# Kernel tuning notes

Measured on AMD Instinct MI355X. Metric: run time of the kernel, lower is better.

## Reference

```python
import jax, jax.numpy as jnp
import numpy as np

WS = 8        # window_size
HEADS = 6     # num_heads
DIM = 96      # dim


def _relative_position_index(ws):
    # Static int index table, identical to the torch buffer construction.
    coords = np.stack(np.meshgrid(np.arange(ws), np.arange(ws), indexing='ij'))  # (2, ws, ws)
    cf = coords.reshape(2, -1)                              # (2, N)
    rel = cf[:, :, None] - cf[:, None, :]                   # (2, N, N)
    rel = rel.transpose(1, 2, 0).copy()                     # (N, N, 2)
    rel[:, :, 0] += ws - 1
    rel[:, :, 1] += ws - 1
    rel[:, :, 0] *= 2 * ws - 1
    return rel.sum(-1)                                      # (N, N)


def setup_inputs() -> dict:
    key = jax.random.key(0)
    ks = jax.random.split(key, 6)
    B, C, H, W = 1, DIM, 512, 512
    return {
        'x': jax.random.normal(ks[0], (B, C, H, W), jnp.float32),
        'qkv_w': jax.random.normal(ks[1], (3 * C, C), jnp.float32) * 0.02,
        'qkv_b': jnp.zeros((3 * C,), jnp.float32),
        'dw_w': jax.random.normal(ks[2], (3 * C, 1, 3, 3), jnp.float32) * 0.02,
        'dw_b': jnp.zeros((3 * C,), jnp.float32),
        'proj_w': jax.random.normal(ks[3], (C, C), jnp.float32) * 0.02,
        'proj_b': jnp.zeros((C,), jnp.float32),
        'temperature': jnp.ones((HEADS, 1, 1), jnp.float32),
        'rel_bias_table': jax.random.normal(ks[4], ((2 * WS - 1) ** 2, HEADS), jnp.float32) * 0.02,
    }


def reference(x, qkv_w, qkv_b, dw_w, dw_b, proj_w, proj_b, temperature, rel_bias_table):
    B, C, H, W = x.shape
    ws, heads = WS, HEADS
    N = ws * ws
    hd = C // heads
    scale = hd ** (-0.5)

    # ---- window partition: (B,C,H,W) -> (B*nW, C, ws, ws) ----
    xw = x.reshape(B, C, H // ws, ws, W // ws, ws)
    xw = xw.transpose(0, 2, 4, 1, 3, 5).reshape(-1, C, ws, ws)

    # ---- qkv 1x1 conv + depthwise 3x3 conv ----
    qkv = jnp.einsum('oi,bihw->bohw', qkv_w, xw) + qkv_b[None, :, None, None]
    qkv = jax.lax.conv_general_dilated(
        qkv, dw_w, window_strides=(1, 1), padding='SAME',
        feature_group_count=3 * C,
        dimension_numbers=('NCHW', 'OIHW', 'NCHW')) + dw_b[None, :, None, None]
    q, k, v = jnp.split(qkv, 3, axis=1)

    # (b, head, c, N)
    def to_heads(t):
        return t.reshape(t.shape[0], heads, hd, N)

    q = to_heads(q * scale)
    k = to_heads(k)
    v = to_heads(v)

    # F.normalize(dim=-1): L2 over the spatial (N) axis, eps=1e-12
    q = q / jnp.clip(jnp.linalg.norm(q, axis=-1, keepdims=True), 1e-12)
    k = k / jnp.clip(jnp.linalg.norm(k, axis=-1, keepdims=True), 1e-12)

    # channel attention: (b,h,c,c)
    attn_ch = jnp.einsum('bhcn,bhdn->bhcd', q, k) * temperature
    # spatial attention: (b,h,N,N)
    attn_sp = jnp.einsum('bhcn,bhcm->bhnm', q, k)

    idx = _relative_position_index(ws).reshape(-1)           # (N*N,)
    bias = rel_bias_table[idx].reshape(N, N, heads).transpose(2, 0, 1)  # (h,N,N)
    attn_sp = attn_sp + bias[None]

    attn_ch = jax.nn.softmax(attn_ch, axis=-1)
    attn_sp = jax.nn.softmax(attn_sp, axis=-1)

    # out = attn_channel @ v @ attn : (b,h,c,N)
    out = jnp.einsum('bhcd,bhdn->bhcn', attn_ch, v)
    out = jnp.einsum('bhcn,bhnm->bhcm', out, attn_sp)

    # back to (B*nW, C, ws, ws) then window reverse -> (B,C,H,W)
    out = out.reshape(-1, C, ws, ws)
    out = out.reshape(B, H // ws, W // ws, C, ws, ws)
    out = out.transpose(0, 3, 1, 4, 2, 5).reshape(B, C, H, W)

    # proj 1x1 conv
    out = jnp.einsum('oi,bihw->bohw', proj_w, out) + proj_b[None, :, None, None]
    return out
```

## Files before the change

kernel.cpp:

```cpp
#include <hip/hip_runtime.h>

typedef short short8 __attribute__((ext_vector_type(8)));
typedef float float4v __attribute__((ext_vector_type(4)));

__device__ __forceinline__ unsigned short f2bf(float f) {
    unsigned int u = __float_as_uint(f);
    u += 0x7fffu + ((u >> 16) & 1u);
    return (unsigned short)(u >> 16);
}
__device__ __forceinline__ float bfs(const unsigned short* p) {
    return __uint_as_float(((unsigned int)*p) << 16);
}
__device__ __forceinline__ float4v mfma16(short8 a, short8 b, float4v c) {
    return __builtin_amdgcn_mfma_f32_16x16x32_bf16(a, b, c, 0, 0, 0);
}

__global__ void prep_pack(const float* __restrict__ qkv_w,
                          const float* __restrict__ proj_w,
                          short* __restrict__ apq, short* __restrict__ app) {
    const int i = blockIdx.x * 256 + threadIdx.x;
    if (i < 3456) {
        const int rem = i % 192, f = rem / 64, lane = rem % 64;
        const int m = (i / 192) * 16 + (lane & 15);
        const int kb = f * 32 + ((lane >> 4) & 3) * 8;
        const float* s = qkv_w + m * 96 + kb;
        short8 o;
        #pragma unroll
        for (int j = 0; j < 8; ++j) o[j] = (short)f2bf(s[j]);
        *(short8*)(apq + i * 8) = o;
    } else if (i < 4608) {
        const int i2 = i - 3456;
        const int rem = i2 % 192, f = rem / 64, lane = rem % 64;
        const int m = (i2 / 192) * 16 + (lane & 15);
        const int kb = f * 32 + ((lane >> 4) & 3) * 8;
        const float* s = proj_w + m * 96 + kb;
        short8 o;
        #pragma unroll
        for (int j = 0; j < 8; ++j) o[j] = (short)f2bf(s[j]);
        *(short8*)(app + i2 * 8) = o;
    }
}

__global__ __launch_bounds__(256, 4)
void fused_win_attn(const float* __restrict__ x,
                    const short* __restrict__ apq,
                    const float* __restrict__ qkv_b,
                    const float* __restrict__ dw_w,
                    const float* __restrict__ dw_b,
                    const short* __restrict__ app,
                    const float* __restrict__ proj_b,
                    const float* __restrict__ temperature,
                    const float* __restrict__ rel_bias,
                    float* __restrict__ yout)
{
    __shared__ __align__(16) unsigned char smem[40080];
    unsigned short* sxT   = (unsigned short*)smem;
    unsigned short* raw   = (unsigned short*)smem;
    unsigned short* sST   = (unsigned short*)smem;
    unsigned short* stmp  = (unsigned short*)(smem + 9216);
    unsigned short* ach   = (unsigned short*)(smem + 11520);
    float*          sred  = (float*)(smem + 12288);
    unsigned short* soutT = (unsigned short*)(smem + 13312);
    unsigned short* sqkv  = (unsigned short*)(smem + 26624);
    unsigned short* qnT   = (unsigned short*)(smem + 31232);
    unsigned short* knT   = (unsigned short*)(smem + 33280);
    unsigned short* vT    = (unsigned short*)(smem + 35328);
    unsigned short* sbias = (unsigned short*)(smem + 37376);

    const int tid  = threadIdx.x;
    const int lane = tid & 63;
    const int g    = tid >> 6;
    const int quad = lane >> 4;
    const int l15  = lane & 15;
    const int wi = blockIdx.x;
    const int y0 = (wi >> 6) << 3;
    const int x0 = (wi & 63) << 3;
    const int py = lane >> 3, px = lane & 7;

    for (int r = tid; r < 1536; r += 256) {
        const int c = r >> 4, p0 = (r & 15) * 4;
        float4 v = *(const float4*)(x + c * 262144 + (y0 + (p0 >> 3)) * 512 + x0 + (p0 & 7));
        sxT[(p0 + 0) * 104 + c] = f2bf(v.x);
        sxT[(p0 + 1) * 104 + c] = f2bf(v.y);
        sxT[(p0 + 2) * 104 + c] = f2bf(v.z);
        sxT[(p0 + 3) * 104 + c] = f2bf(v.w);
    }
    for (int r = tid; r < 1350; r += 256) sbias[r] = f2bf(rel_bias[r]);
    __syncthreads();

    short8 bfx[3];
    #pragma unroll
    for (int f = 0; f < 3; ++f)
        bfx[f] = *(const short8*)(sxT + (g * 16 + l15) * 104 + f * 32 + quad * 8);
    __syncthreads();

    for (int h = 0; h < 6; ++h) {
        for (int r = tid; r < 1728; r += 256) {
            const int ch = r / 36, k = r % 36;
            int cell;
            if (k < 10)      cell = k;
            else if (k < 20) cell = 90 + (k - 10);
            else if (k < 28) cell = (k - 19) * 10;
            else             cell = (k - 27) * 10 + 9;
            raw[ch * 100 + cell] = 0;
        }
        {
            const int p = g * 16 + l15;
            const int wcell = (p >> 3) * 10 + (p & 7) + 11;
            #pragma unroll
            for (int t = 0; t < 3; ++t) {
                float4v acc = {0.f, 0.f, 0.f, 0.f};
                #pragma unroll
                for (int f = 0; f < 3; ++f) {
                    short8 af = *(const short8*)(apq + (((t * 6 + h) * 3 + f) * 64 + lane) * 8);
                    acc = mfma16(af, bfx[f], acc);
                }
                #pragma unroll
                for (int reg = 0; reg < 4; ++reg) {
                    const int rr = quad * 4 + reg;
                    raw[(t * 16 + rr) * 100 + wcell] =
                        f2bf(acc[reg] + qkv_b[t * 96 + h * 16 + rr]);
                }
            }
        }
        __syncthreads();

        {
            unsigned int qw0 = 0, qw1 = 0, kw0 = 0, kw1 = 0, vw0 = 0, vw1 = 0;
            #pragma unroll
            for (int r = 0; r < 12; ++r) {
                const int j = (r >> 2) * 16 + 4 * g + (r & 3);
                const int O = __builtin_amdgcn_readfirstlane((j >> 4) * 96 + h * 16 + (j & 15));
                const float* wq = dw_w + O * 9;
                float a = dw_b[O];
                const unsigned short* rbase = raw + j * 100 + py * 10 + px;
                a = fmaf(wq[0], bfs(rbase +  0), a);
                a = fmaf(wq[1], bfs(rbase +  1), a);
                a = fmaf(wq[2], bfs(rbase +  2), a);
                a = fmaf(wq[3], bfs(rbase + 10), a);
                a = fmaf(wq[4], bfs(rbase + 11), a);
                a = fmaf(wq[5], bfs(rbase + 12), a);
                a = fmaf(wq[6], bfs(rbase + 20), a);
                a = fmaf(wq[7], bfs(rbase + 21), a);
                a = fmaf(wq[8], bfs(rbase + 22), a);
                if (r < 8) {
                    float ss = a * a;
                    #pragma unroll
                    for (int m = 1; m < 64; m <<= 1) ss += __shfl_xor(ss, m, 64);
                    a = a * (1.f / fmaxf(sqrtf(ss), 1e-12f));
                    sqkv[j * 72 + lane] = f2bf(a);
                }
                const unsigned int bv = f2bf(a);
                if      (r == 0)  qw0 |= bv;          else if (r == 1)  qw0 |= bv << 16;
                else if (r == 2)  qw1 |= bv;          else if (r == 3)  qw1 |= bv << 16;
                else if (r == 4)  kw0 |= bv;          else if (r == 5)  kw0 |= bv << 16;
                else if (r == 6)  kw1 |= bv;          else if (r == 7)  kw1 |= bv << 16;
                else if (r == 8)  vw0 |= bv;          else if (r == 9)  vw0 |= bv << 16;
                else if (r == 10) vw1 |= bv;          else              vw1 |= bv << 16;
            }
            uint2 uq; uq.x = qw0; uq.y = qw1;
            uint2 uk; uk.x = kw0; uk.y = kw1;
            uint2 uv; uv.x = vw0; uv.y = vw1;
            *(uint2*)(qnT + lane * 16 + 4 * g) = uq;
            *(uint2*)(knT + lane * 16 + 4 * g) = uk;
            *(uint2*)(vT  + lane * 16 + 4 * g) = uv;
        }
        __syncthreads();

        {
            short8 ak = {0, 0, 0, 0, 0, 0, 0, 0};
            if (lane < 32) ak = *(const short8*)(knT + (g * 16 + l15) * 16 + quad * 8);
            #pragma unroll
            for (int nt = 0; nt < 4; ++nt) {
                short8 bq = {0, 0, 0, 0, 0, 0, 0, 0};
                if (lane < 32) bq = *(const short8*)(qnT + (nt * 16 + l15) * 16 + quad * 8);
                float4v cs = {0.f, 0.f, 0.f, 0.f};
                cs = mfma16(ak, bq, cs);
                float ps = 0.f;
                #pragma unroll
                for (int reg = 0; reg < 4; ++reg) {
                    const int m = g * 16 + quad * 4 + reg;
                    const int n = nt * 16 + l15;
                    const int idx = ((n >> 3) - (m >> 3) + 7) * 15 + ((n & 7) - (m & 7) + 7);
                    const float e = __expf(cs[reg] + bfs(sbias + idx * 6 + h));
                    sST[m * 72 + n] = f2bf(e);
                    ps += e;
                }
                ps += __shfl_xor(ps, 16, 64);
                ps += __shfl_xor(ps, 32, 64);
                if (lane < 16) sred[g * 64 + nt * 16 + lane] = ps;
            }
        }
        if (g == 0) {
            short8 a0 = *(const short8*)(sqkv + l15 * 72 + quad * 8);
            short8 a1 = *(const short8*)(sqkv + l15 * 72 + 32 + quad * 8);
            short8 b0 = *(const short8*)(sqkv + (16 + l15) * 72 + quad * 8);
            short8 b1 = *(const short8*)(sqkv + (16 + l15) * 72 + 32 + quad * 8);
            float4v cc = {0.f, 0.f, 0.f, 0.f};
            cc = mfma16(a0, b0, cc);
            cc = mfma16(a1, b1, cc);
            const float tp = temperature[h];
            #pragma unroll
            for (int reg = 0; reg < 4; ++reg) {
                const float e = __expf(cc[reg] * tp);
                float se = e;
                #pragma unroll
                for (int m = 1; m < 16; m <<= 1) se += __shfl_xor(se, m, 64);
                ach[(quad * 4 + reg) * 24 + l15] = f2bf(e / se);
            }
        }
        __syncthreads();

        {
            const int n = g * 16 + l15;
            const float inv = 1.f / (sred[n] + sred[64 + n] + sred[128 + n] + sred[192 + n]);
            short8 af = {0, 0, 0, 0, 0, 0, 0, 0}, bv = {0, 0, 0, 0, 0, 0, 0, 0};
            if (lane < 32) {
                af = *(const short8*)(ach + l15 * 24 + quad * 8);
                bv = *(const short8*)(vT + (g * 16 + l15) * 16 + quad * 8);
            }
            float4v ct = {0.f, 0.f, 0.f, 0.f};
            ct = mfma16(af, bv, ct);
            #pragma unroll
            for (int reg = 0; reg < 4; ++reg)
                stmp[(quad * 4 + reg) * 72 + g * 16 + l15] = f2bf(ct[reg] * inv);
        }
        __syncthreads();

        {
            short8 a0 = *(const short8*)(stmp + l15 * 72 + quad * 8);
            short8 a1 = *(const short8*)(stmp + l15 * 72 + 32 + quad * 8);
            short8 b0 = *(const short8*)(sST + (g * 16 + l15) * 72 + quad * 8);
            short8 b1 = *(const short8*)(sST + (g * 16 + l15) * 72 + 32 + quad * 8);
            float4v co = {0.f, 0.f, 0.f, 0.f};
            co = mfma16(a0, b0, co);
            co = mfma16(a1, b1, co);
            #pragma unroll
            for (int reg = 0; reg < 4; ++reg)
                soutT[(g * 16 + l15) * 104 + h * 16 + quad * 4 + reg] = f2bf(co[reg]);
        }
        __syncthreads();
    }

    {
        short8 pb[3];
        #pragma unroll
        for (int f = 0; f < 3; ++f)
            pb[f] = *(const short8*)(soutT + (g * 16 + l15) * 104 + f * 32 + quad * 8);
        const int p = g * 16 + l15;
        float* outbase = yout + (y0 + (p >> 3)) * 512 + x0 + (p & 7);
        #pragma unroll
        for (int mt = 0; mt < 6; ++mt) {
            float4v acc = {0.f, 0.f, 0.f, 0.f};
            #pragma unroll
            for (int f = 0; f < 3; ++f) {
                short8 af = *(const short8*)(app + ((mt * 3 + f) * 64 + lane) * 8);
                acc = mfma16(af, pb[f], acc);
            }
            #pragma unroll
            for (int reg = 0; reg < 4; ++reg) {
                const int o = mt * 16 + quad * 4 + reg;
                outbase[o * 262144] = acc[reg] + proj_b[o];
            }
        }
    }
}

extern "C" void kernel_launch(void* const* d_in, const int* in_sizes, int n_in,
                              void* d_out, int out_size, void* d_ws, size_t ws_size,
                              hipStream_t stream) {
    const float* x      = (const float*)d_in[0];
    const float* qkv_w  = (const float*)d_in[1];
    const float* qkv_b  = (const float*)d_in[2];
    const float* dw_w   = (const float*)d_in[3];
    const float* dw_b   = (const float*)d_in[4];
    const float* proj_w = (const float*)d_in[5];
    const float* proj_b = (const float*)d_in[6];
    const float* temp   = (const float*)d_in[7];
    const float* relb   = (const float*)d_in[8];
    float* o = (float*)d_out;

    short* apq = (short*)d_ws;
    short* app = apq + 27648;

    hipLaunchKernelGGL(prep_pack, dim3(18), dim3(256), 0, stream, qkv_w, proj_w, apq, app);
    hipLaunchKernelGGL(fused_win_attn, dim3(4096), dim3(256), 0, stream,
                       x, apq, qkv_b, dw_w, dw_b, app, proj_b, temp, relb, o);
}
```

Baseline: 644.8 us.

## Shrink LDS footprint, fuse projection per head pair, swizzle shared buffers

Shared memory per block drops from about 40KB to 32KB and launch bounds rise to 5 blocks per SIMD, aiming for higher occupancy. Instead of a full 96-channel output staging buffer, the projection MFMA is accumulated in registers after every pair of heads. The spatial softmax row sums are now kept in registers, which removes the sred buffer. Padded strides, an XOR swizzle and split 64-bit loads are added to cut LDS bank conflicts. In exchange the kernel holds 24 more accumulator registers, which risks spills under the tighter register limit, and it changes the schedule of the MFMA work.

```diff
diff --git a/kernel.cpp b/kernel.cpp
--- a/kernel.cpp
+++ b/kernel.cpp
@@ -2,6 +2,7 @@
 
 typedef short short8 __attribute__((ext_vector_type(8)));
 typedef float float4v __attribute__((ext_vector_type(4)));
+typedef unsigned int uint2v __attribute__((ext_vector_type(2)));
 
 __device__ __forceinline__ unsigned short f2bf(float f) {
     unsigned int u = __float_as_uint(f);
@@ -13,6 +14,12 @@
 }
 __device__ __forceinline__ float4v mfma16(short8 a, short8 b, float4v c) {
     return __builtin_amdgcn_mfma_f32_16x16x32_bf16(a, b, c, 0, 0, 0);
+}
+__device__ __forceinline__ short8 ld_b64x2(const unsigned short* p) {
+    union { short8 s; uint2v u[2]; } r;
+    r.u[0] = *(const uint2v*)(p);
+    r.u[1] = *(const uint2v*)(p + 4);
+    return r.s;
 }
 
 __global__ void prep_pack(const float* __restrict__ qkv_w,
@@ -41,7 +48,7 @@
     }
 }
 
-__global__ __launch_bounds__(256, 4)
+__global__ __launch_bounds__(256, 5)
 void fused_win_attn(const float* __restrict__ x,
                     const short* __restrict__ apq,
                     const float* __restrict__ qkv_b,
@@ -53,19 +60,18 @@
                     const float* __restrict__ rel_bias,
                     float* __restrict__ yout)
 {
-    __shared__ __align__(16) unsigned char smem[40080];
+    __shared__ __align__(16) unsigned char smem[32400];
     unsigned short* sxT   = (unsigned short*)smem;
     unsigned short* raw   = (unsigned short*)smem;
     unsigned short* sST   = (unsigned short*)smem;
-    unsigned short* stmp  = (unsigned short*)(smem + 9216);
-    unsigned short* ach   = (unsigned short*)(smem + 11520);
-    float*          sred  = (float*)(smem + 12288);
-    unsigned short* soutT = (unsigned short*)(smem + 13312);
-    unsigned short* sqkv  = (unsigned short*)(smem + 26624);
-    unsigned short* qnT   = (unsigned short*)(smem + 31232);
-    unsigned short* knT   = (unsigned short*)(smem + 33280);
-    unsigned short* vT    = (unsigned short*)(smem + 35328);
-    unsigned short* sbias = (unsigned short*)(smem + 37376);
+    unsigned short* stmp  = (unsigned short*)(smem + 9728);
+    unsigned short* ach   = (unsigned short*)(smem + 12160);
+    unsigned short* sqkv  = (unsigned short*)(smem + 13312);
+    unsigned short* qnT   = (unsigned short*)(smem + 17408);
+    unsigned short* knT   = (unsigned short*)(smem + 19968);
+    unsigned short* vT    = (unsigned short*)(smem + 22528);
+    unsigned short* sbias = (unsigned short*)(smem + 25088);
+    unsigned short* outT  = (unsigned short*)(smem + 27792);
 
     const int tid  = threadIdx.x;
     const int lane = tid & 63;
@@ -94,19 +100,22 @@
         bfx[f] = *(const short8*)(sxT + (g * 16 + l15) * 104 + f * 32 + quad * 8);
     __syncthreads();
 
+    float4v yacc[6];
+    #pragma unroll
+    for (int mt = 0; mt < 6; ++mt) yacc[mt] = (float4v){0.f, 0.f, 0.f, 0.f};
+
     for (int h = 0; h < 6; ++h) {
-        for (int r = tid; r < 1728; r += 256) {
-            const int ch = r / 36, k = r % 36;
+        for (int r = tid; r < 1296; r += 256) {
+            const int ch = r / 27, k = r % 27;
             int cell;
-            if (k < 10)      cell = k;
-            else if (k < 20) cell = 90 + (k - 10);
-            else if (k < 28) cell = (k - 19) * 10;
-            else             cell = (k - 27) * 10 + 9;
-            raw[ch * 100 + cell] = 0;
+            if (k < 9)       cell = k;
+            else if (k < 18) cell = (k - 8) * 9;
+            else             cell = 82 + (k - 18);
+            raw[ch * 91 + cell] = 0;
         }
         {
             const int p = g * 16 + l15;
-            const int wcell = (p >> 3) * 10 + (p & 7) + 11;
+            const int wcell = (p >> 3) * 9 + (p & 7) + 10;
             #pragma unroll
             for (int t = 0; t < 3; ++t) {
                 float4v acc = {0.f, 0.f, 0.f, 0.f};
@@ -118,7 +127,7 @@
                 #pragma unroll
                 for (int reg = 0; reg < 4; ++reg) {
                     const int rr = quad * 4 + reg;
-                    raw[(t * 16 + rr) * 100 + wcell] =
+                    raw[(t * 16 + rr) * 91 + wcell] =
                         f2bf(acc[reg] + qkv_b[t * 96 + h * 16 + rr]);
                 }
             }
@@ -133,22 +142,22 @@
                 const int O = __builtin_amdgcn_readfirstlane((j >> 4) * 96 + h * 16 + (j & 15));
                 const float* wq = dw_w + O * 9;
                 float a = dw_b[O];
-                const unsigned short* rbase = raw + j * 100 + py * 10 + px;
+                const unsigned short* rbase = raw + j * 91 + py * 9 + px;
                 a = fmaf(wq[0], bfs(rbase +  0), a);
                 a = fmaf(wq[1], bfs(rbase +  1), a);
                 a = fmaf(wq[2], bfs(rbase +  2), a);
-                a = fmaf(wq[3], bfs(rbase + 10), a);
-                a = fmaf(wq[4], bfs(rbase + 11), a);
-                a = fmaf(wq[5], bfs(rbase + 12), a);
-                a = fmaf(wq[6], bfs(rbase + 20), a);
-                a = fmaf(wq[7], bfs(rbase + 21), a);
-                a = fmaf(wq[8], bfs(rbase + 22), a);
+                a = fmaf(wq[3], bfs(rbase +  9), a);
+                a = fmaf(wq[4], bfs(rbase + 10), a);
+                a = fmaf(wq[5], bfs(rbase + 11), a);
+                a = fmaf(wq[6], bfs(rbase + 18), a);
+                a = fmaf(wq[7], bfs(rbase + 19), a);
+                a = fmaf(wq[8], bfs(rbase + 20), a);
                 if (r < 8) {
                     float ss = a * a;
                     #pragma unroll
                     for (int m = 1; m < 64; m <<= 1) ss += __shfl_xor(ss, m, 64);
                     a = a * (1.f / fmaxf(sqrtf(ss), 1e-12f));
-                    sqkv[j * 72 + lane] = f2bf(a);
+                    sqkv[j * 64 + (lane ^ ((j & 7) * 8))] = f2bf(a);
                 }
                 const unsigned int bv = f2bf(a);
                 if      (r == 0)  qw0 |= bv;          else if (r == 1)  qw0 |= bv << 16;
@@ -158,44 +167,44 @@
                 else if (r == 8)  vw0 |= bv;          else if (r == 9)  vw0 |= bv << 16;
                 else if (r == 10) vw1 |= bv;          else              vw1 |= bv << 16;
             }
-            uint2 uq; uq.x = qw0; uq.y = qw1;
-            uint2 uk; uk.x = kw0; uk.y = kw1;
-            uint2 uv; uv.x = vw0; uv.y = vw1;
-            *(uint2*)(qnT + lane * 16 + 4 * g) = uq;
-            *(uint2*)(knT + lane * 16 + 4 * g) = uk;
-            *(uint2*)(vT  + lane * 16 + 4 * g) = uv;
-        }
-        __syncthreads();
-
-        {
-            short8 ak = {0, 0, 0, 0, 0, 0, 0, 0};
-            if (lane < 32) ak = *(const short8*)(knT + (g * 16 + l15) * 16 + quad * 8);
-            #pragma unroll
-            for (int nt = 0; nt < 4; ++nt) {
-                short8 bq = {0, 0, 0, 0, 0, 0, 0, 0};
-                if (lane < 32) bq = *(const short8*)(qnT + (nt * 16 + l15) * 16 + quad * 8);
+            uint2v uq; uq.x = qw0; uq.y = qw1;
+            uint2v uk; uk.x = kw0; uk.y = kw1;
+            uint2v uv; uv.x = vw0; uv.y = vw1;
+            *(uint2v*)(qnT + lane * 20 + 4 * g) = uq;
+            *(uint2v*)(knT + lane * 20 + 4 * g) = uk;
+            *(uint2v*)(vT  + lane * 20 + 4 * g) = uv;
+        }
+        __syncthreads();
+
+        float lsum = 0.f;
+        {
+            short8 bq = {0, 0, 0, 0, 0, 0, 0, 0};
+            if (lane < 32) bq = ld_b64x2(qnT + (g * 16 + l15) * 20 + quad * 8);
+            #pragma unroll
+            for (int mt = 0; mt < 4; ++mt) {
+                short8 ak = {0, 0, 0, 0, 0, 0, 0, 0};
+                if (lane < 32) ak = ld_b64x2(knT + (mt * 16 + l15) * 20 + quad * 8);
                 float4v cs = {0.f, 0.f, 0.f, 0.f};
                 cs = mfma16(ak, bq, cs);
-                float ps = 0.f;
                 #pragma unroll
                 for (int reg = 0; reg < 4; ++reg) {
-                    const int m = g * 16 + quad * 4 + reg;
-                    const int n = nt * 16 + l15;
+                    const int m = mt * 16 + quad * 4 + reg;
+                    const int n = g * 16 + l15;
                     const int idx = ((n >> 3) - (m >> 3) + 7) * 15 + ((n & 7) - (m & 7) + 7);
                     const float e = __expf(cs[reg] + bfs(sbias + idx * 6 + h));
-                    sST[m * 72 + n] = f2bf(e);
-                    ps += e;
-                }
-                ps += __shfl_xor(ps, 16, 64);
-                ps += __shfl_xor(ps, 32, 64);
-                if (lane < 16) sred[g * 64 + nt * 16 + lane] = ps;
-            }
+                    sST[m * 76 + n] = f2bf(e);
+                    lsum += e;
+                }
+            }
+            lsum += __shfl_xor(lsum, 16, 64);
+            lsum += __shfl_xor(lsum, 32, 64);
         }
         if (g == 0) {
-            short8 a0 = *(const short8*)(sqkv + l15 * 72 + quad * 8);
-            short8 a1 = *(const short8*)(sqkv + l15 * 72 + 32 + quad * 8);
-            short8 b0 = *(const short8*)(sqkv + (16 + l15) * 72 + quad * 8);
-            short8 b1 = *(const short8*)(sqkv + (16 + l15) * 72 + 32 + quad * 8);
+            const int sw = (l15 & 7) * 8;
+            short8 a0 = *(const short8*)(sqkv + l15 * 64 + ((quad * 8) ^ sw));
+            short8 a1 = *(const short8*)(sqkv + l15 * 64 + (((quad + 4) * 8) ^ sw));
+            short8 b0 = *(const short8*)(sqkv + (16 + l15) * 64 + ((quad * 8) ^ sw));
+            short8 b1 = *(const short8*)(sqkv + (16 + l15) * 64 + (((quad + 4) * 8) ^ sw));
             float4v cc = {0.f, 0.f, 0.f, 0.f};
             cc = mfma16(a0, b0, cc);
             cc = mfma16(a1, b1, cc);
@@ -212,55 +221,54 @@
         __syncthreads();
 
         {
-            const int n = g * 16 + l15;
-            const float inv = 1.f / (sred[n] + sred[64 + n] + sred[128 + n] + sred[192 + n]);
+            const float inv = 1.f / lsum;
             short8 af = {0, 0, 0, 0, 0, 0, 0, 0}, bv = {0, 0, 0, 0, 0, 0, 0, 0};
             if (lane < 32) {
                 af = *(const short8*)(ach + l15 * 24 + quad * 8);
-                bv = *(const short8*)(vT + (g * 16 + l15) * 16 + quad * 8);
+                bv = ld_b64x2(vT + (g * 16 + l15) * 20 + quad * 8);
             }
             float4v ct = {0.f, 0.f, 0.f, 0.f};
             ct = mfma16(af, bv, ct);
             #pragma unroll
             for (int reg = 0; reg < 4; ++reg)
-                stmp[(quad * 4 + reg) * 72 + g * 16 + l15] = f2bf(ct[reg] * inv);
-        }
-        __syncthreads();
-
-        {
-            short8 a0 = *(const short8*)(stmp + l15 * 72 + quad * 8);
-            short8 a1 = *(const short8*)(stmp + l15 * 72 + 32 + quad * 8);
-            short8 b0 = *(const short8*)(sST + (g * 16 + l15) * 72 + quad * 8);
-            short8 b1 = *(const short8*)(sST + (g * 16 + l15) * 72 + 32 + quad * 8);
+                stmp[(quad * 4 + reg) * 76 + g * 16 + l15] = f2bf(ct[reg] * inv);
+        }
+        __syncthreads();
+
+        {
+            short8 a0 = ld_b64x2(stmp + l15 * 76 + quad * 8);
+            short8 a1 = ld_b64x2(stmp + l15 * 76 + 32 + quad * 8);
+            short8 b0 = ld_b64x2(sST + (g * 16 + l15) * 76 + quad * 8);
+            short8 b1 = ld_b64x2(sST + (g * 16 + l15) * 76 + 32 + quad * 8);
             float4v co = {0.f, 0.f, 0.f, 0.f};
             co = mfma16(a0, b0, co);
             co = mfma16(a1, b1, co);
             #pragma unroll
             for (int reg = 0; reg < 4; ++reg)
-                soutT[(g * 16 + l15) * 104 + h * 16 + quad * 4 + reg] = f2bf(co[reg]);
-        }
-        __syncthreads();
+                outT[(g * 16 + l15) * 36 + (h & 1) * 16 + quad * 4 + reg] = f2bf(co[reg]);
+        }
+        __syncthreads();
+
+        if (h & 1) {
+            const int hp = h >> 1;
+            short8 bo = ld_b64x2(outT + (g * 16 + l15) * 36 + quad * 8);
+            #pragma unroll
+            for (int mt = 0; mt < 6; ++mt) {
+                short8 af = *(const short8*)(app + ((mt * 3 + hp) * 64 + lane) * 8);
+                yacc[mt] = mfma16(af, bo, yacc[mt]);
+            }
+        }
     }
 
     {
-        short8 pb[3];
-        #pragma unroll
-        for (int f = 0; f < 3; ++f)
-            pb[f] = *(const short8*)(soutT + (g * 16 + l15) * 104 + f * 32 + quad * 8);
         const int p = g * 16 + l15;
         float* outbase = yout + (y0 + (p >> 3)) * 512 + x0 + (p & 7);
         #pragma unroll
         for (int mt = 0; mt < 6; ++mt) {
-            float4v acc = {0.f, 0.f, 0.f, 0.f};
-            #pragma unroll
-            for (int f = 0; f < 3; ++f) {
-                short8 af = *(const short8*)(app + ((mt * 3 + f) * 64 + lane) * 8);
-                acc = mfma16(af, pb[f], acc);
-            }
             #pragma unroll
             for (int reg = 0; reg < 4; ++reg) {
                 const int o = mt * 16 + quad * 4 + reg;
-                outbase[o * 262144] = acc[reg] + proj_b[o];
+                outbase[o * 262144] = yacc[mt][reg] + proj_b[o];
             }
         }
     }
```

New measurement: 857.9 us. 1.33x slower.
